# Kernel optimization log

Measured on AMD Instinct MI355X. Metric: run time of the kernel, lower is better.

Reference implementation:

```python
import jax, jax.numpy as jnp
import numpy as np

N = 100000   # nodes
E = 3200000  # edges (avg degree 32)
F = 10       # input features
H = 20       # hidden dim
G = 512      # graphs in batch
L = 2        # labels


def xavier(key, shape):
    fan_in, fan_out = shape[0], shape[1]
    a = jnp.sqrt(6.0 / (fan_in + fan_out))
    return jax.random.uniform(key, shape, jnp.float32, -a, a)


def setup_inputs() -> dict:
    key = jax.random.key(0)
    ks = jax.random.split(key, 12)
    x = jax.random.normal(ks[0], (N, F), jnp.float32)
    edge_index = jax.random.randint(ks[1], (2, E), 0, N, jnp.int64)
    batch = jnp.sort(jax.random.randint(ks[2], (N,), 0, G, jnp.int64))
    return {
        "x": x,
        "edge_index": edge_index,
        "batch": batch,
        # layer 1: F -> H
        "W_rel1": xavier(ks[3], (F, H)), "b1": jnp.zeros((H,), jnp.float32),
        "W_root1": xavier(ks[4], (F, H)),
        # layer 2: H -> H
        "W_rel2": xavier(ks[5], (H, H)), "b2": jnp.zeros((H,), jnp.float32),
        "W_root2": xavier(ks[6], (H, H)),
        # layer 3: H -> H
        "W_rel3": xavier(ks[7], (H, H)), "b3": jnp.zeros((H,), jnp.float32),
        "W_root3": xavier(ks[8], (H, H)),
        # readout linear: 2H -> L
        "W_lin": xavier(ks[9], (2 * H, L)), "b_lin": jnp.zeros((L,), jnp.float32),
    }


def _graph_conv(x, src, dst, W_rel, b, W_root):
    # PyG GraphConv: out = lin_rel(sum_{j->i} x_j) + lin_root(x_i)
    agg = jax.ops.segment_sum(x[src], dst, num_segments=N)  # [N, d_in]
    return agg @ W_rel + b + x @ W_root


def reference(x, edge_index, batch, W_rel1, b1, W_root1, W_rel2, b2, W_root2,
              W_rel3, b3, W_root3, W_lin, b_lin):
    src, dst = edge_index[0], edge_index[1]
    h = jax.nn.relu(_graph_conv(x, src, dst, W_rel1, b1, W_root1))
    h = jax.nn.relu(_graph_conv(h, src, dst, W_rel2, b2, W_root2))
    h = jax.nn.relu(_graph_conv(h, src, dst, W_rel3, b3, W_root3))  # [N, H]
    # global max / mean pool over graphs
    maxp = jax.ops.segment_max(h, batch, num_segments=G)            # [G, H]
    sump = jax.ops.segment_sum(h, batch, num_segments=G)            # [G, H]
    counts = jax.ops.segment_sum(jnp.ones((h.shape[0], 1), h.dtype), batch,
                                 num_segments=G)                    # [G, 1]
    nonempty = counts > 0
    maxp = jnp.where(nonempty, maxp, 0.0)
    meanp = sump / jnp.maximum(counts, 1.0)
    pooled = jnp.concatenate([maxp, meanp], axis=-1)                # [G, 2H]
    return pooled @ W_lin + b_lin
```

## Files before the change

kernel.cpp:

```cpp
#include <hip/hip_runtime.h>
#include <hip/hip_bf16.h>

#define NN 100000
#define FF 10
#define HH 20
#define GG 512
#define LL 2

#define NB 500
#define BNODES 200
#define CAP 7168
#define HB 100
#define SCAP 3712
#define TILE 4096
#define SRC_BITS 17
#define SRC_MASK 0x1FFFFu

__device__ inline unsigned short f2bf(float f) {
  unsigned u = __float_as_uint(f);
  unsigned r = u + 0x7FFFu + ((u >> 16) & 1u);
  return (unsigned short)(r >> 16);
}
__device__ inline float bflo(unsigned u) { return __uint_as_float(u << 16); }
__device__ inline float bfhi(unsigned u) { return __uint_as_float(u & 0xFFFF0000u); }

__global__ __launch_bounds__(256) void cast_init_kernel(
    const float* __restrict__ x, unsigned short* __restrict__ xb,
    float* __restrict__ sump, int* __restrict__ maxp, float* __restrict__ cnt,
    int* __restrict__ cursor, int n) {
  int i = blockIdx.x * 256 + threadIdx.x;
  if (i < n) xb[i] = f2bf(__builtin_nontemporal_load(x + i));
  if (i < GG * HH) {
    sump[i] = 0.0f;
    maxp[i] = 0;
  }
  if (i < GG) cnt[i] = 0.0f;
  if (i < NB) cursor[i] = 0;
}

__global__ __launch_bounds__(512) void multisplit_kernel(
    const int* __restrict__ src, const int* __restrict__ dst,
    int* __restrict__ cursor, unsigned int* __restrict__ pay, int E) {
  __shared__ int lhist[NB];
  __shared__ int lofs[NB];
  __shared__ int gbase[NB];
  __shared__ int lcur[NB];
  __shared__ unsigned int sord[TILE];
  __shared__ unsigned short sdbk[TILE];
  __shared__ int ss[512];
  int t = threadIdx.x;
  if (t < NB) lhist[t] = 0;
  __syncthreads();

  int base = blockIdx.x * TILE;
  int count = E - base;
  if (count > TILE) count = TILE;

  for (int i = t; i < count; i += 512)
    atomicAdd(&lhist[dst[base + i] / BNODES], 1);
  __syncthreads();

  int own = (t < NB) ? lhist[t] : 0;
  ss[t] = own;
  __syncthreads();
  for (int off = 1; off < 512; off <<= 1) {
    int a0 = (t >= off) ? ss[t - off] : 0;
    __syncthreads();
    ss[t] += a0;
    __syncthreads();
  }
  if (t < NB) {
    lofs[t] = ss[t] - own;
    int bo = own ? atomicAdd(&cursor[t], own) : 0;
    if (bo > CAP - own) bo = CAP - own;
    gbase[t] = t * CAP + bo;
    lcur[t] = 0;
  }
  __syncthreads();

  for (int i = t; i < count; i += 512) {
    int e = base + i;
    int d = __builtin_nontemporal_load(dst + e);
    int s = __builtin_nontemporal_load(src + e);
    int bk = d / BNODES;
    int ld = d - bk * BNODES;
    int r = atomicAdd(&lcur[bk], 1);
    int slot = lofs[bk] + r;
    sord[slot] = ((unsigned)ld << SRC_BITS) | (unsigned)s;
    sdbk[slot] = (unsigned short)bk;
  }
  __syncthreads();

  for (int i = t; i < count; i += 512) {
    int bk = sdbk[i];
    pay[gbase[bk] + (i - lofs[bk])] = sord[i];
  }
}

__global__ __launch_bounds__(256) void bucket_csr_kernel(
    const unsigned int* __restrict__ pay, const int* __restrict__ cursor,
    int* __restrict__ srt, int* __restrict__ rofs, int* __restrict__ rend) {
  __shared__ int lhist[BNODES];
  __shared__ int lofs[BNODES];
  __shared__ int lcur[BNODES];
  __shared__ int ss[256];
  int b = blockIdx.x;
  int t = threadIdx.x;
  int k0 = b * CAP;
  int ecnt = cursor[b];
  if (ecnt > CAP) ecnt = CAP;

  if (t < BNODES) lhist[t] = 0;
  __syncthreads();
  for (int k = t; k < ecnt; k += 256)
    atomicAdd(&lhist[pay[k0 + k] >> SRC_BITS], 1);
  __syncthreads();

  int own = (t < BNODES) ? lhist[t] : 0;
  ss[t] = own;
  __syncthreads();
  for (int off = 1; off < 256; off <<= 1) {
    int a0 = (t >= off) ? ss[t - off] : 0;
    __syncthreads();
    ss[t] += a0;
    __syncthreads();
  }
  if (t < BNODES) {
    int ex = ss[t] - own;
    lofs[t] = ex;
    lcur[t] = 0;
    rofs[b * BNODES + t] = k0 + ex;
    rend[b * BNODES + t] = k0 + ex + own;
  }
  __syncthreads();

  for (int k = t; k < ecnt; k += 256) {
    unsigned p = pay[k0 + k];
    int ld = p >> SRC_BITS;
    int r = atomicAdd(&lcur[ld], 1);
    srt[k0 + lofs[ld] + r] = (int)(p & SRC_MASK);
  }
}

template<int DIN>
__global__ __launch_bounds__(512) void bucket_layer_kernel(
    const unsigned short* __restrict__ hin, const int* __restrict__ srt,
    const int* __restrict__ rofs, const int* __restrict__ rend,
    const float* __restrict__ Wrel, const float* __restrict__ bias,
    const float* __restrict__ Wroot, unsigned short* __restrict__ hout) {
  constexpr int AST = (DIN == 10) ? 11 : 21;
  constexpr int CH = DIN / 5;
  __shared__ int sSrc[SCAP];
  __shared__ float acc[HB * AST];
  __shared__ unsigned short roots[HB * DIN];
  __shared__ float sWrel[DIN * HH];
  __shared__ float sWroot[DIN * HH];
  __shared__ float sb[HH];
  __shared__ int sRofs[HB];
  __shared__ int sRend[HB];
  __shared__ int sSeg0, sSegLen;
  int b2 = blockIdx.x;
  int t = threadIdx.x;
  int nbase = b2 * HB;

  for (int i = t; i < DIN * HH; i += 512) {
    sWrel[i] = Wrel[i];
    sWroot[i] = Wroot[i];
  }
  if (t < HH) sb[t] = bias[t];
  if (t < HB) {
    sRofs[t] = rofs[nbase + t];
    sRend[t] = rend[nbase + t];
  }
  if (t == 0) {
    int s0 = rofs[nbase];
    int sl = rend[nbase + HB - 1] - s0;
    sSeg0 = s0;
    sSegLen = sl < SCAP ? sl : SCAP;
  }
  {
    const unsigned* rs = (const unsigned*)(hin + (size_t)nbase * DIN);
    unsigned* rd = (unsigned*)roots;
    for (int i = t; i < HB * DIN / 2; i += 512) rd[i] = rs[i];
  }
  __syncthreads();

  int seg0 = sSeg0, seglen = sSegLen;
  for (int i = t; i < seglen; i += 512) sSrc[i] = srt[seg0 + i];
  __syncthreads();

  if (t < HB * 5) {
    int ln = t / 5;
    int c = t - ln * 5;
    int k0 = sRofs[ln] - seg0;
    int k1 = sRend[ln] - seg0;
    if (k1 > seglen) k1 = seglen;
    float a0 = 0, a1 = 0, a2 = 0, a3 = 0;
    const unsigned short* xb = hin + c * CH;
    if (CH == 4) {
      for (int k = k0; k < k1; k++) {
        uint2 u = *(const uint2*)(xb + (size_t)sSrc[k] * DIN);
        a0 += bflo(u.x);
        a1 += bfhi(u.x);
        a2 += bflo(u.y);
        a3 += bfhi(u.y);
      }
    } else {
      for (int k = k0; k < k1; k++) {
        unsigned u = *(const unsigned*)(xb + (size_t)sSrc[k] * DIN);
        a0 += bflo(u);
        a1 += bfhi(u);
      }
    }
    float* a = acc + ln * AST + c * CH;
    if (CH == 4) {
      a[0] = a0; a[1] = a1; a[2] = a2; a[3] = a3;
    } else {
      a[0] = a0; a[1] = a1;
    }
  }
  __syncthreads();

  for (int idx = t; idx < HB * HH; idx += 512) {
    int ln = idx / HH;
    int j = idx - ln * HH;
    const float* a = acc + ln * AST;
    const unsigned short* r = roots + ln * DIN;
    float v = sb[j];
#pragma unroll
    for (int f = 0; f < DIN; f++) {
      v += a[f] * sWrel[f * HH + j];
      v += bflo((unsigned)r[f]) * sWroot[f * HH + j];
    }
    hout[(size_t)nbase * HH + idx] = f2bf(fmaxf(v, 0.0f));
  }
}

__global__ __launch_bounds__(512) void bucket_layer_pool_kernel(
    const unsigned short* __restrict__ hin, const int* __restrict__ srt,
    const int* __restrict__ rofs, const int* __restrict__ rend,
    const float* __restrict__ Wrel, const float* __restrict__ bias,
    const float* __restrict__ Wroot, const int* __restrict__ batch,
    float* __restrict__ sump, int* __restrict__ maxp,
    float* __restrict__ cnt) {
  constexpr int DIN = 20;
  constexpr int AST = 21;
  __shared__ int sSrc[SCAP];
  __shared__ float acc[HB * AST];
  __shared__ unsigned short roots[HB * DIN];
  __shared__ int sBatch[HB];
  __shared__ float sWrel[DIN * HH];
  __shared__ float sWroot[DIN * HH];
  __shared__ float sb[HH];
  __shared__ int sRofs[HB];
  __shared__ int sRend[HB];
  __shared__ int sSeg0, sSegLen;
  int b2 = blockIdx.x;
  int t = threadIdx.x;
  int nbase = b2 * HB;

  for (int i = t; i < DIN * HH; i += 512) {
    sWrel[i] = Wrel[i];
    sWroot[i] = Wroot[i];
  }
  if (t < HH) sb[t] = bias[t];
  if (t < HB) {
    sRofs[t] = rofs[nbase + t];
    sRend[t] = rend[nbase + t];
    sBatch[t] = batch[nbase + t];
  }
  if (t == 0) {
    int s0 = rofs[nbase];
    int sl = rend[nbase + HB - 1] - s0;
    sSeg0 = s0;
    sSegLen = sl < SCAP ? sl : SCAP;
  }
  {
    const unsigned* rs = (const unsigned*)(hin + (size_t)nbase * DIN);
    unsigned* rd = (unsigned*)roots;
    for (int i = t; i < HB * DIN / 2; i += 512) rd[i] = rs[i];
  }
  __syncthreads();

  int seg0 = sSeg0, seglen = sSegLen;
  for (int i = t; i < seglen; i += 512) sSrc[i] = srt[seg0 + i];
  __syncthreads();

  if (t < HB * 5) {
    int ln = t / 5;
    int c = t - ln * 5;
    int k0 = sRofs[ln] - seg0;
    int k1 = sRend[ln] - seg0;
    if (k1 > seglen) k1 = seglen;
    float a0 = 0, a1 = 0, a2 = 0, a3 = 0;
    const unsigned short* xb = hin + c * 4;
    for (int k = k0; k < k1; k++) {
      uint2 u = *(const uint2*)(xb + (size_t)sSrc[k] * 20);
      a0 += bflo(u.x);
      a1 += bfhi(u.x);
      a2 += bflo(u.y);
      a3 += bfhi(u.y);
    }
    float* a = acc + ln * AST + c * 4;
    a[0] = a0; a[1] = a1; a[2] = a2; a[3] = a3;
  }
  __syncthreads();

  float vreg[4];
#pragma unroll
  for (int u = 0; u < 4; u++) {
    int idx = t + u * 512;
    if (idx < HB * HH) {
      int ln = idx / HH;
      int j = idx - ln * HH;
      const float* a = acc + ln * AST;
      const unsigned short* r = roots + ln * DIN;
      float v = sb[j];
#pragma unroll
      for (int f = 0; f < DIN; f++) {
        v += a[f] * sWrel[f * HH + j];
        v += bflo((unsigned)r[f]) * sWroot[f * HH + j];
      }
      vreg[u] = fmaxf(v, 0.0f);
    }
  }
  __syncthreads();
#pragma unroll
  for (int u = 0; u < 4; u++) {
    int idx = t + u * 512;
    if (idx < HB * HH) {
      int ln = idx / HH;
      int j = idx - ln * HH;
      acc[ln * AST + j] = vreg[u];
    }
  }
  __syncthreads();

  int g0 = sBatch[0];
  int g1 = sBatch[HB - 1];
  int ngr = g1 - g0 + 1;
  for (int it = t; it < ngr * HH; it += 512) {
    int gi = it / HH;
    int j = it - gi * HH;
    int g = g0 + gi;
    float s = 0.0f, m = 0.0f;
    int c = 0;
    for (int ln = 0; ln < HB; ln++) {
      if (sBatch[ln] == g) {
        float v = acc[ln * AST + j];
        s += v;
        m = fmaxf(m, v);
        c++;
      }
    }
    if (c) {
      atomicAdd(&sump[g * HH + j], s);
      atomicMax(&maxp[g * HH + j], __float_as_int(m));
      if (j == 0) atomicAdd(&cnt[g], (float)c);
    }
  }
}

__global__ __launch_bounds__(256) void readout_kernel(
    const float* __restrict__ sump, const int* __restrict__ maxp,
    const float* __restrict__ cnt, const float* __restrict__ Wlin,
    const float* __restrict__ blin, float* __restrict__ out) {
  int idx = blockIdx.x * 256 + threadIdx.x;
  if (idx >= GG * LL) return;
  int g = idx / LL;
  int l = idx - g * LL;
  float c = cnt[g];
  float inv = 1.0f / fmaxf(c, 1.0f);
  float acc = blin[l];
#pragma unroll
  for (int j = 0; j < HH; j++) {
    float mx = __int_as_float(maxp[g * HH + j]);
    float mean = sump[g * HH + j] * inv;
    acc += mx * Wlin[j * LL + l];
    acc += mean * Wlin[(HH + j) * LL + l];
  }
  out[idx] = acc;
}

extern "C" void kernel_launch(void* const* d_in, const int* in_sizes, int n_in,
                              void* d_out, int out_size, void* d_ws,
                              size_t ws_size, hipStream_t stream) {
  const float* x = (const float*)d_in[0];
  const int* edge_index = (const int*)d_in[1];
  const int* batch = (const int*)d_in[2];
  const float* W_rel1 = (const float*)d_in[3];
  const float* b1 = (const float*)d_in[4];
  const float* W_root1 = (const float*)d_in[5];
  const float* W_rel2 = (const float*)d_in[6];
  const float* b2 = (const float*)d_in[7];
  const float* W_root2 = (const float*)d_in[8];
  const float* W_rel3 = (const float*)d_in[9];
  const float* b3 = (const float*)d_in[10];
  const float* W_root3 = (const float*)d_in[11];
  const float* W_lin = (const float*)d_in[12];
  const float* b_lin = (const float*)d_in[13];
  float* out = (float*)d_out;

  const int E = in_sizes[1] / 2;
  const int n_nodes = in_sizes[0] / FF;
  const int* src = edge_index;
  const int* dst = edge_index + E;

  unsigned int* pay = (unsigned int*)d_ws;
  int* srt = (int*)(pay + (size_t)NB * CAP);
  int* rofs = srt + (size_t)NB * CAP;
  int* rend = rofs + NN;
  int* cursor = rend + NN;
  float* sump = (float*)(cursor + 512);
  int* maxp = (int*)(sump + GG * HH);
  float* cnt = (float*)(maxp + GG * HH);
  unsigned short* xb = (unsigned short*)(cnt + 512);
  unsigned short* h1 = xb + (size_t)NN * FF;
  unsigned short* h2 = h1 + (size_t)NN * HH;

  const int edge_tiles = (E + TILE - 1) / TILE;

  cast_init_kernel<<<(n_nodes * FF + 255) / 256, 256, 0, stream>>>(
      x, xb, sump, maxp, cnt, cursor, n_nodes * FF);

  multisplit_kernel<<<edge_tiles, 512, 0, stream>>>(src, dst, cursor, pay, E);
  bucket_csr_kernel<<<NB, 256, 0, stream>>>(pay, cursor, srt, rofs, rend);

  bucket_layer_kernel<FF><<<NB * 2, 512, 0, stream>>>(
      xb, srt, rofs, rend, W_rel1, b1, W_root1, h1);
  bucket_layer_kernel<HH><<<NB * 2, 512, 0, stream>>>(
      h1, srt, rofs, rend, W_rel2, b2, W_root2, h2);
  bucket_layer_pool_kernel<<<NB * 2, 512, 0, stream>>>(
      h2, srt, rofs, rend, W_rel3, b3, W_root3, batch, sump, maxp, cnt);

  readout_kernel<<<(GG * LL + 255) / 256, 256, 0, stream>>>(
      sump, maxp, cnt, W_lin, b_lin, out);
}
```

Baseline: 261.6 us.

## Split node features into aligned column planes for 16-byte gathers

Node feature arrays are stored as separate planes (8+2 columns for the input, 8+8+4 for hidden layers) instead of packed rows of 10 or 20 bf16 values. Each neighbor gather then uses aligned 16-byte (uint4) loads with fewer threads per node (2 or 3 instead of 5), cutting the number of load instructions per edge. The epilogue writes two outputs per thread as packed 32-bit stores into the planes. The cost is more index arithmetic in the cast and root staging, and the gather work is spread over fewer threads, so each gathering thread does more per edge.

Result: slower. 311.8 us (+19.2%).

```diff
diff --git a/kernel.cpp b/kernel.cpp
--- a/kernel.cpp
+++ b/kernel.cpp
@@ -25,11 +25,19 @@
 __device__ inline float bfhi(unsigned u) { return __uint_as_float(u & 0xFFFF0000u); }
 
 __global__ __launch_bounds__(256) void cast_init_kernel(
-    const float* __restrict__ x, unsigned short* __restrict__ xb,
-    float* __restrict__ sump, int* __restrict__ maxp, float* __restrict__ cnt,
-    int* __restrict__ cursor, int n) {
+    const float* __restrict__ x, unsigned short* __restrict__ xA,
+    unsigned short* __restrict__ xB, float* __restrict__ sump,
+    int* __restrict__ maxp, float* __restrict__ cnt, int* __restrict__ cursor) {
   int i = blockIdx.x * 256 + threadIdx.x;
-  if (i < n) xb[i] = f2bf(__builtin_nontemporal_load(x + i));
+  if (i < NN * FF) {
+    int n = i / FF;
+    int f = i - n * FF;
+    unsigned short v = f2bf(__builtin_nontemporal_load(x + i));
+    if (f < 8)
+      xA[n * 8 + f] = v;
+    else
+      xB[n * 2 + (f - 8)] = v;
+  }
   if (i < GG * HH) {
     sump[i] = 0.0f;
     maxp[i] = 0;
@@ -142,14 +150,15 @@
   }
 }
 
-template<int DIN>
-__global__ __launch_bounds__(512) void bucket_layer_kernel(
-    const unsigned short* __restrict__ hin, const int* __restrict__ srt,
-    const int* __restrict__ rofs, const int* __restrict__ rend,
-    const float* __restrict__ Wrel, const float* __restrict__ bias,
-    const float* __restrict__ Wroot, unsigned short* __restrict__ hout) {
-  constexpr int AST = (DIN == 10) ? 11 : 21;
-  constexpr int CH = DIN / 5;
+__global__ __launch_bounds__(512) void layer1_kernel(
+    const unsigned short* __restrict__ xA, const unsigned short* __restrict__ xB,
+    const int* __restrict__ srt, const int* __restrict__ rofs,
+    const int* __restrict__ rend, const float* __restrict__ Wrel,
+    const float* __restrict__ bias, const float* __restrict__ Wroot,
+    unsigned short* __restrict__ hA, unsigned short* __restrict__ hB,
+    unsigned short* __restrict__ hC) {
+  constexpr int DIN = 10;
+  constexpr int AST = 11;
   __shared__ int sSrc[SCAP];
   __shared__ float acc[HB * AST];
   __shared__ unsigned short roots[HB * DIN];
@@ -179,9 +188,12 @@
     sSegLen = sl < SCAP ? sl : SCAP;
   }
   {
-    const unsigned* rs = (const unsigned*)(hin + (size_t)nbase * DIN);
-    unsigned* rd = (unsigned*)roots;
-    for (int i = t; i < HB * DIN / 2; i += 512) rd[i] = rs[i];
+    unsigned* rootsU = (unsigned*)roots;
+    const unsigned* aU = (const unsigned*)xA + (size_t)nbase * 4;
+    const unsigned* bU = (const unsigned*)xB + (size_t)nbase;
+    for (int i = t; i < HB * 4; i += 512)
+      rootsU[(i >> 2) * 5 + (i & 3)] = aU[i];
+    for (int i = t; i < HB; i += 512) rootsU[i * 5 + 4] = bU[i];
   }
   __syncthreads();
 
@@ -189,55 +201,195 @@
   for (int i = t; i < seglen; i += 512) sSrc[i] = srt[seg0 + i];
   __syncthreads();
 
-  if (t < HB * 5) {
-    int ln = t / 5;
-    int c = t - ln * 5;
+  if (t < HB * 2) {
+    int ln = t >> 1;
+    int c = t & 1;
     int k0 = sRofs[ln] - seg0;
     int k1 = sRend[ln] - seg0;
     if (k1 > seglen) k1 = seglen;
-    float a0 = 0, a1 = 0, a2 = 0, a3 = 0;
-    const unsigned short* xb = hin + c * CH;
-    if (CH == 4) {
+    if (c == 0) {
+      float a0 = 0, a1 = 0, a2 = 0, a3 = 0, a4 = 0, a5 = 0, a6 = 0, a7 = 0;
+      const uint4* p = (const uint4*)xA;
       for (int k = k0; k < k1; k++) {
-        uint2 u = *(const uint2*)(xb + (size_t)sSrc[k] * DIN);
-        a0 += bflo(u.x);
-        a1 += bfhi(u.x);
-        a2 += bflo(u.y);
-        a3 += bfhi(u.y);
+        uint4 u = p[sSrc[k]];
+        a0 += bflo(u.x); a1 += bfhi(u.x);
+        a2 += bflo(u.y); a3 += bfhi(u.y);
+        a4 += bflo(u.z); a5 += bfhi(u.z);
+        a6 += bflo(u.w); a7 += bfhi(u.w);
       }
+      float* a = acc + ln * AST;
+      a[0] = a0; a[1] = a1; a[2] = a2; a[3] = a3;
+      a[4] = a4; a[5] = a5; a[6] = a6; a[7] = a7;
     } else {
+      float a0 = 0, a1 = 0;
+      const unsigned* p = (const unsigned*)xB;
       for (int k = k0; k < k1; k++) {
-        unsigned u = *(const unsigned*)(xb + (size_t)sSrc[k] * DIN);
+        unsigned u = p[sSrc[k]];
         a0 += bflo(u);
         a1 += bfhi(u);
       }
-    }
-    float* a = acc + ln * AST + c * CH;
-    if (CH == 4) {
-      a[0] = a0; a[1] = a1; a[2] = a2; a[3] = a3;
-    } else {
+      float* a = acc + ln * AST + 8;
       a[0] = a0; a[1] = a1;
     }
   }
   __syncthreads();
 
-  for (int idx = t; idx < HB * HH; idx += 512) {
-    int ln = idx / HH;
-    int j = idx - ln * HH;
+  unsigned* hAU = (unsigned*)hA;
+  unsigned* hBU = (unsigned*)hB;
+  unsigned* hCU = (unsigned*)hC;
+  for (int idx = t; idx < HB * 10; idx += 512) {
+    int ln = idx / 10;
+    int ju = idx - ln * 10;
+    int j0 = ju * 2;
     const float* a = acc + ln * AST;
     const unsigned short* r = roots + ln * DIN;
-    float v = sb[j];
+    float v0 = sb[j0], v1 = sb[j0 + 1];
 #pragma unroll
     for (int f = 0; f < DIN; f++) {
-      v += a[f] * sWrel[f * HH + j];
-      v += bflo((unsigned)r[f]) * sWroot[f * HH + j];
-    }
-    hout[(size_t)nbase * HH + idx] = f2bf(fmaxf(v, 0.0f));
-  }
-}
-
-__global__ __launch_bounds__(512) void bucket_layer_pool_kernel(
-    const unsigned short* __restrict__ hin, const int* __restrict__ srt,
+      float av = a[f];
+      float rv = bflo((unsigned)r[f]);
+      v0 += av * sWrel[f * HH + j0] + rv * sWroot[f * HH + j0];
+      v1 += av * sWrel[f * HH + j0 + 1] + rv * sWroot[f * HH + j0 + 1];
+    }
+    unsigned outv = (unsigned)f2bf(fmaxf(v0, 0.0f)) |
+                    ((unsigned)f2bf(fmaxf(v1, 0.0f)) << 16);
+    int n = nbase + ln;
+    if (ju < 4)
+      hAU[(size_t)n * 4 + ju] = outv;
+    else if (ju < 8)
+      hBU[(size_t)n * 4 + (ju - 4)] = outv;
+    else
+      hCU[(size_t)n * 2 + (ju - 8)] = outv;
+  }
+}
+
+#define STAGE_H_ROOTS(hA_, hB_, hC_)                                       \
+  {                                                                        \
+    unsigned* rootsU = (unsigned*)roots;                                   \
+    const unsigned* aU = (const unsigned*)(hA_) + (size_t)nbase * 4;       \
+    const unsigned* bU = (const unsigned*)(hB_) + (size_t)nbase * 4;       \
+    const unsigned* cU = (const unsigned*)(hC_) + (size_t)nbase * 2;       \
+    for (int i = t; i < HB * 4; i += 512)                                  \
+      rootsU[(i >> 2) * 10 + (i & 3)] = aU[i];                             \
+    for (int i = t; i < HB * 4; i += 512)                                  \
+      rootsU[(i >> 2) * 10 + 4 + (i & 3)] = bU[i];                         \
+    for (int i = t; i < HB * 2; i += 512)                                  \
+      rootsU[(i >> 1) * 10 + 8 + (i & 1)] = cU[i];                         \
+  }
+
+#define GATHER_H_SPLIT(hA_, hB_, hC_)                                      \
+  if (t < HB * 3) {                                                        \
+    int ln = t / 3;                                                        \
+    int c = t - ln * 3;                                                    \
+    int k0 = sRofs[ln] - seg0;                                             \
+    int k1 = sRend[ln] - seg0;                                             \
+    if (k1 > seglen) k1 = seglen;                                          \
+    if (c < 2) {                                                           \
+      const uint4* p = (const uint4*)(c == 0 ? (hA_) : (hB_));             \
+      float a0 = 0, a1 = 0, a2 = 0, a3 = 0, a4 = 0, a5 = 0, a6 = 0,        \
+            a7 = 0;                                                        \
+      for (int k = k0; k < k1; k++) {                                      \
+        uint4 u = p[sSrc[k]];                                              \
+        a0 += bflo(u.x); a1 += bfhi(u.x);                                  \
+        a2 += bflo(u.y); a3 += bfhi(u.y);                                  \
+        a4 += bflo(u.z); a5 += bfhi(u.z);                                  \
+        a6 += bflo(u.w); a7 += bfhi(u.w);                                  \
+      }                                                                    \
+      float* a = acc + ln * AST + c * 8;                                   \
+      a[0] = a0; a[1] = a1; a[2] = a2; a[3] = a3;                          \
+      a[4] = a4; a[5] = a5; a[6] = a6; a[7] = a7;                          \
+    } else {                                                               \
+      const uint2* p = (const uint2*)(hC_);                                \
+      float a0 = 0, a1 = 0, a2 = 0, a3 = 0;                                \
+      for (int k = k0; k < k1; k++) {                                      \
+        uint2 u = p[sSrc[k]];                                              \
+        a0 += bflo(u.x); a1 += bfhi(u.x);                                  \
+        a2 += bflo(u.y); a3 += bfhi(u.y);                                  \
+      }                                                                    \
+      float* a = acc + ln * AST + 16;                                      \
+      a[0] = a0; a[1] = a1; a[2] = a2; a[3] = a3;                          \
+    }                                                                      \
+  }
+
+__global__ __launch_bounds__(512) void layer2_kernel(
+    const unsigned short* __restrict__ iA, const unsigned short* __restrict__ iB,
+    const unsigned short* __restrict__ iC, const int* __restrict__ srt,
+    const int* __restrict__ rofs, const int* __restrict__ rend,
+    const float* __restrict__ Wrel, const float* __restrict__ bias,
+    const float* __restrict__ Wroot, unsigned short* __restrict__ oA,
+    unsigned short* __restrict__ oB, unsigned short* __restrict__ oC) {
+  constexpr int DIN = 20;
+  constexpr int AST = 21;
+  __shared__ int sSrc[SCAP];
+  __shared__ float acc[HB * AST];
+  __shared__ unsigned short roots[HB * DIN];
+  __shared__ float sWrel[DIN * HH];
+  __shared__ float sWroot[DIN * HH];
+  __shared__ float sb[HH];
+  __shared__ int sRofs[HB];
+  __shared__ int sRend[HB];
+  __shared__ int sSeg0, sSegLen;
+  int b2 = blockIdx.x;
+  int t = threadIdx.x;
+  int nbase = b2 * HB;
+
+  for (int i = t; i < DIN * HH; i += 512) {
+    sWrel[i] = Wrel[i];
+    sWroot[i] = Wroot[i];
+  }
+  if (t < HH) sb[t] = bias[t];
+  if (t < HB) {
+    sRofs[t] = rofs[nbase + t];
+    sRend[t] = rend[nbase + t];
+  }
+  if (t == 0) {
+    int s0 = rofs[nbase];
+    int sl = rend[nbase + HB - 1] - s0;
+    sSeg0 = s0;
+    sSegLen = sl < SCAP ? sl : SCAP;
+  }
+  STAGE_H_ROOTS(iA, iB, iC)
+  __syncthreads();
+
+  int seg0 = sSeg0, seglen = sSegLen;
+  for (int i = t; i < seglen; i += 512) sSrc[i] = srt[seg0 + i];
+  __syncthreads();
+
+  GATHER_H_SPLIT(iA, iB, iC)
+  __syncthreads();
+
+  unsigned* hAU = (unsigned*)oA;
+  unsigned* hBU = (unsigned*)oB;
+  unsigned* hCU = (unsigned*)oC;
+  for (int idx = t; idx < HB * 10; idx += 512) {
+    int ln = idx / 10;
+    int ju = idx - ln * 10;
+    int j0 = ju * 2;
+    const float* a = acc + ln * AST;
+    const unsigned short* r = roots + ln * DIN;
+    float v0 = sb[j0], v1 = sb[j0 + 1];
+#pragma unroll
+    for (int f = 0; f < DIN; f++) {
+      float av = a[f];
+      float rv = bflo((unsigned)r[f]);
+      v0 += av * sWrel[f * HH + j0] + rv * sWroot[f * HH + j0];
+      v1 += av * sWrel[f * HH + j0 + 1] + rv * sWroot[f * HH + j0 + 1];
+    }
+    unsigned outv = (unsigned)f2bf(fmaxf(v0, 0.0f)) |
+                    ((unsigned)f2bf(fmaxf(v1, 0.0f)) << 16);
+    int n = nbase + ln;
+    if (ju < 4)
+      hAU[(size_t)n * 4 + ju] = outv;
+    else if (ju < 8)
+      hBU[(size_t)n * 4 + (ju - 4)] = outv;
+    else
+      hCU[(size_t)n * 2 + (ju - 8)] = outv;
+  }
+}
+
+__global__ __launch_bounds__(512) void layer3_pool_kernel(
+    const unsigned short* __restrict__ iA, const unsigned short* __restrict__ iB,
+    const unsigned short* __restrict__ iC, const int* __restrict__ srt,
     const int* __restrict__ rofs, const int* __restrict__ rend,
     const float* __restrict__ Wrel, const float* __restrict__ bias,
     const float* __restrict__ Wroot, const int* __restrict__ batch,
@@ -275,35 +427,14 @@
     sSeg0 = s0;
     sSegLen = sl < SCAP ? sl : SCAP;
   }
-  {
-    const unsigned* rs = (const unsigned*)(hin + (size_t)nbase * DIN);
-    unsigned* rd = (unsigned*)roots;
-    for (int i = t; i < HB * DIN / 2; i += 512) rd[i] = rs[i];
-  }
+  STAGE_H_ROOTS(iA, iB, iC)
   __syncthreads();
 
   int seg0 = sSeg0, seglen = sSegLen;
   for (int i = t; i < seglen; i += 512) sSrc[i] = srt[seg0 + i];
   __syncthreads();
 
-  if (t < HB * 5) {
-    int ln = t / 5;
-    int c = t - ln * 5;
-    int k0 = sRofs[ln] - seg0;
-    int k1 = sRend[ln] - seg0;
-    if (k1 > seglen) k1 = seglen;
-    float a0 = 0, a1 = 0, a2 = 0, a3 = 0;
-    const unsigned short* xb = hin + c * 4;
-    for (int k = k0; k < k1; k++) {
-      uint2 u = *(const uint2*)(xb + (size_t)sSrc[k] * 20);
-      a0 += bflo(u.x);
-      a1 += bfhi(u.x);
-      a2 += bflo(u.y);
-      a3 += bfhi(u.y);
-    }
-    float* a = acc + ln * AST + c * 4;
-    a[0] = a0; a[1] = a1; a[2] = a2; a[3] = a3;
-  }
+  GATHER_H_SPLIT(iA, iB, iC)
   __syncthreads();
 
   float vreg[4];
@@ -402,7 +533,6 @@
   float* out = (float*)d_out;
 
   const int E = in_sizes[1] / 2;
-  const int n_nodes = in_sizes[0] / FF;
   const int* src = edge_index;
   const int* dst = edge_index + E;
 
@@ -414,24 +544,30 @@
   float* sump = (float*)(cursor + 512);
   int* maxp = (int*)(sump + GG * HH);
   float* cnt = (float*)(maxp + GG * HH);
-  unsigned short* xb = (unsigned short*)(cnt + 512);
-  unsigned short* h1 = xb + (size_t)NN * FF;
-  unsigned short* h2 = h1 + (size_t)NN * HH;
+  unsigned short* xA = (unsigned short*)(cnt + 512);
+  unsigned short* xB = xA + (size_t)NN * 8;
+  unsigned short* h1A = xB + (size_t)NN * 2;
+  unsigned short* h1B = h1A + (size_t)NN * 8;
+  unsigned short* h1C = h1B + (size_t)NN * 8;
+  unsigned short* h2A = h1C + (size_t)NN * 4;
+  unsigned short* h2B = h2A + (size_t)NN * 8;
+  unsigned short* h2C = h2B + (size_t)NN * 8;
 
   const int edge_tiles = (E + TILE - 1) / TILE;
 
-  cast_init_kernel<<<(n_nodes * FF + 255) / 256, 256, 0, stream>>>(
-      x, xb, sump, maxp, cnt, cursor, n_nodes * FF);
+  cast_init_kernel<<<(NN * FF + 255) / 256, 256, 0, stream>>>(
+      x, xA, xB, sump, maxp, cnt, cursor);
 
   multisplit_kernel<<<edge_tiles, 512, 0, stream>>>(src, dst, cursor, pay, E);
   bucket_csr_kernel<<<NB, 256, 0, stream>>>(pay, cursor, srt, rofs, rend);
 
-  bucket_layer_kernel<FF><<<NB * 2, 512, 0, stream>>>(
-      xb, srt, rofs, rend, W_rel1, b1, W_root1, h1);
-  bucket_layer_kernel<HH><<<NB * 2, 512, 0, stream>>>(
-      h1, srt, rofs, rend, W_rel2, b2, W_root2, h2);
-  bucket_layer_pool_kernel<<<NB * 2, 512, 0, stream>>>(
-      h2, srt, rofs, rend, W_rel3, b3, W_root3, batch, sump, maxp, cnt);
+  layer1_kernel<<<NB * 2, 512, 0, stream>>>(
+      xA, xB, srt, rofs, rend, W_rel1, b1, W_root1, h1A, h1B, h1C);
+  layer2_kernel<<<NB * 2, 512, 0, stream>>>(
+      h1A, h1B, h1C, srt, rofs, rend, W_rel2, b2, W_root2, h2A, h2B, h2C);
+  layer3_pool_kernel<<<NB * 2, 512, 0, stream>>>(
+      h2A, h2B, h2C, srt, rofs, rend, W_rel3, b3, W_root3, batch, sump, maxp,
+      cnt);
 
   readout_kernel<<<(GG * LL + 255) / 256, 256, 0, stream>>>(
       sump, maxp, cnt, W_lin, b_lin, out);
```
